# Optimization experiments

Hardware: AMD Instinct MI355X
Metric: run time of the kernel (lower is better)

The kernel has to match this reference:

```python
import jax, jax.numpy as jnp
import numpy as np

SENT_LEN, SENT_BATCH, WORD_LEN = 256, 64, 16
EMB, HID = 128, 256
CEMB, CHID = 64, 128
VOCAB, CVOCAB, TAGS = 50000, 128, 50


def setup_inputs() -> dict:
    key = jax.random.key(0)
    ks = jax.random.split(key, 14)
    s = 0.1  # param init scale, avoids gate saturation
    n = lambda k, shape: (jax.random.normal(k, shape, dtype=jnp.float32) * s)
    return {
        "sentences": jax.random.randint(ks[0], (SENT_LEN, SENT_BATCH), 0, VOCAB),
        "words": jax.random.randint(ks[1], (SENT_BATCH, WORD_LEN, SENT_LEN), 0, CVOCAB),
        "char_embedding_dim": CEMB,
        "char_hidden_dim": CHID,
        "word_emb": n(ks[2], (VOCAB, EMB)),
        "char_emb": n(ks[3], (CVOCAB, CEMB)),
        "Wih_c": n(ks[4], (4 * CHID, CEMB)),
        "Whh_c": n(ks[5], (4 * CHID, CHID)),
        "bih_c": n(ks[6], (4 * CHID,)),
        "bhh_c": n(ks[7], (4 * CHID,)),
        "Wih_w": n(ks[8], (4 * HID, EMB + CHID)),
        "Whh_w": n(ks[9], (4 * HID, HID)),
        "bih_w": n(ks[10], (4 * HID,)),
        "bhh_w": n(ks[11], (4 * HID,)),
        "W_tag": n(ks[12], (TAGS, HID)),
        "b_tag": n(ks[13], (TAGS,)),
    }


def _lstm_cell(h, c, x, Wih, Whh, b):
    # torch gate order: input, forget, cell(g), output
    gates = x @ Wih.T + h @ Whh.T + b
    i, f, g, o = jnp.split(gates, 4, axis=-1)
    c_new = jax.nn.sigmoid(f) * c + jax.nn.sigmoid(i) * jnp.tanh(g)
    h_new = jax.nn.sigmoid(o) * jnp.tanh(c_new)
    return h_new, c_new


def reference(sentences, words, char_embedding_dim, char_hidden_dim,
              word_emb, char_emb, Wih_c, Whh_c, bih_c, bhh_c,
              Wih_w, Whh_w, bih_w, bhh_w, W_tag, b_tag):
    sent_len, sent_batch = sentences.shape
    dt = word_emb.dtype

    embeds = word_emb[sentences]            # [T, B, EMB]
    ce = char_emb[words]                    # [B, WL, T, CEMB]

    # char LSTM: per sentence, seq=WL, batch=T; hidden carried ACROSS sentences
    b_c = bih_c + bhh_c

    def char_sentence(carry, sent_ce):      # sent_ce: [WL, T, CEMB]
        def step(hc, x):
            h, c = _lstm_cell(hc[0], hc[1], x, Wih_c, Whh_c, b_c)
            return (h, c), None
        carry, _ = jax.lax.scan(step, carry, sent_ce)
        return carry, carry[0]               # final h: [T, CHID]

    init_c = (jnp.zeros((sent_len, CHID), dt), jnp.zeros((sent_len, CHID), dt))
    _, char_finals = jax.lax.scan(char_sentence, init_c, ce)  # [B, T, CHID]
    char_finals = jnp.transpose(char_finals, (1, 0, 2))        # [T, B, CHID]

    x = jnp.concatenate([embeds, char_finals], axis=-1)        # [T, B, EMB+CHID]

    # word LSTM over time=T, batch=B
    b_w = bih_w + bhh_w

    def word_step(hc, xt):
        h, c = _lstm_cell(hc[0], hc[1], xt, Wih_w, Whh_w, b_w)
        return (h, c), h

    init_w = (jnp.zeros((sent_batch, HID), dt), jnp.zeros((sent_batch, HID), dt))
    _, lstm_out = jax.lax.scan(word_step, init_w, x)           # [T, B, HID]

    tag_space = lstm_out @ W_tag.T + b_tag                     # [T, B, TAGS]
    return jax.nn.log_softmax(tag_space, axis=-1)
```

## Files before the change

kernel.cpp:

```cpp
#include <hip/hip_runtime.h>
#include <hip/hip_bf16.h>
#include <cstdint>

#define SENT_LEN   256
#define SENT_BATCH 64
#define WORD_LEN   16
#define EMB        128
#define HID        256
#define CEMB       64
#define CHID       128
#define TAGS       50
#define K_IN       (EMB + CHID)
#define LOG2E      1.44269504f
#define N2LOG2E    -2.88539008f

typedef __attribute__((ext_vector_type(8))) short short8;
typedef __attribute__((ext_vector_type(4))) float f32x4;
typedef __attribute__((ext_vector_type(4))) int   i32x4;
typedef __attribute__((ext_vector_type(2))) long  lng2;

__device__ __forceinline__ float rcpf(float x) { return __builtin_amdgcn_rcpf(x); }
__device__ __forceinline__ float sig2(float xl) {
    return rcpf(1.f + __builtin_amdgcn_exp2f(-xl));
}
__device__ __forceinline__ float tanh2(float xl) {
    float e = __builtin_amdgcn_exp2f(-(xl + xl));
    return 2.f * rcpf(1.f + e) - 1.f;
}
__device__ __forceinline__ float lstm_act(float gi, float gf, float gg, float go, float& cst) {
    float c = sig2(gf) * cst + sig2(gi) * tanh2(gg);
    cst = c;
    float tc = 2.f * rcpf(1.f + __builtin_amdgcn_exp2f(N2LOG2E * c)) - 1.f;
    return sig2(go) * tc;
}
__device__ __forceinline__ float bf_lo(unsigned u) { return __uint_as_float(u << 16); }
__device__ __forceinline__ float bf_hi(unsigned u) { return __uint_as_float(u & 0xffff0000u); }
__device__ __forceinline__ unsigned short f2bfu(float f) {
    unsigned u = __float_as_uint(f);
    u += 0x7fff + ((u >> 16) & 1);
    return (unsigned short)(u >> 16);
}
__device__ __forceinline__ void block_sync_lds() {
    asm volatile("s_waitcnt lgkmcnt(0)\ns_barrier" ::: "memory");
}
__device__ __forceinline__ i32x4 mfma_i8_k64(lng2 a, lng2 b, i32x4 c) {
    c = __builtin_amdgcn_mfma_i32_16x16x32_i8(a.x, b.x, c, 0, 0, 0);
    return __builtin_amdgcn_mfma_i32_16x16x32_i8(a.y, b.y, c, 0, 0, 0);
}

__global__ void prep_char(const float* __restrict__ Wih_c, const float* __restrict__ char_emb,
                          const float* __restrict__ bih_c, const float* __restrict__ bhh_c,
                          float* __restrict__ pre8) {
    int ch = blockIdx.x;
    int g  = threadIdx.x;
    float acc = bih_c[g] + bhh_c[g];
    const float* w = Wih_c + g * CEMB;
    const float* e = char_emb + ch * CEMB;
#pragma unroll
    for (int k = 0; k < CEMB; k++) acc += w[k] * e[k];
    int gt = g >> 7, j = g & 127;
    pre8[((ch * 128) + j) * 4 + gt] = acc * LOG2E;
}

__global__ void prep_wq(const float* __restrict__ Whh_w, signed char* __restrict__ wq,
                        float* __restrict__ sw) {
    int g = blockIdx.x;
    int lane = threadIdx.x;
    float4 v = reinterpret_cast<const float4*>(Whh_w + (size_t)g * HID)[lane];
    float m = fmaxf(fmaxf(fabsf(v.x), fabsf(v.y)), fmaxf(fabsf(v.z), fabsf(v.w)));
#pragma unroll
    for (int off = 32; off; off >>= 1) m = fmaxf(m, __shfl_xor(m, off, 64));
    m = fmaxf(m, 1e-20f);
    float inv = 127.f / m;
    int q0 = __float2int_rn(v.x * inv), q1 = __float2int_rn(v.y * inv);
    int q2 = __float2int_rn(v.z * inv), q3 = __float2int_rn(v.w * inv);
    int packed = (q0 & 255) | ((q1 & 255) << 8) | ((q2 & 255) << 16) | ((q3 & 255) << 24);
    reinterpret_cast<int*>(wq)[g * 64 + lane] = packed;
    if (lane == 0) sw[g] = m / 127.f;
}

__global__ __launch_bounds__(512, 1) void char_lstm(
        const int* __restrict__ words, const float* __restrict__ Whh_c,
        const float* __restrict__ pre8, float* __restrict__ cf) {
    int t    = blockIdx.x;
    int tid  = threadIdx.x;
    int lane = tid & 63, w = tid >> 6;
    int l15  = lane & 15, lq = lane >> 4;
    int j    = w * 16 + l15;

    __shared__ __align__(16) signed char hv[2][128];

    lng2 bfr[4][2];
    float swl[4];
#pragma unroll
    for (int nt = 0; nt < 4; nt++) {
        const float* wr = Whh_c + (size_t)(nt * 128 + j) * CHID;
        float v[2][16];
        float m = 0.f;
#pragma unroll
        for (int kt = 0; kt < 2; kt++) {
#pragma unroll
            for (int q = 0; q < 4; q++) {
                float4 f = reinterpret_cast<const float4*>(wr + kt * 64 + lq * 16 + q * 4)[0];
                v[kt][q * 4 + 0] = f.x; v[kt][q * 4 + 1] = f.y;
                v[kt][q * 4 + 2] = f.z; v[kt][q * 4 + 3] = f.w;
            }
#pragma unroll
            for (int p = 0; p < 16; p++) m = fmaxf(m, fabsf(v[kt][p]));
        }
        m = fmaxf(m, __shfl_xor(m, 16, 64));
        m = fmaxf(m, __shfl_xor(m, 32, 64));
        m = fmaxf(m, 1e-20f);
        float inv = 127.f / m;
#pragma unroll
        for (int kt = 0; kt < 2; kt++) {
            unsigned long lo = 0, hi = 0;
#pragma unroll
            for (int p = 0; p < 8; p++) {
                lo |= (unsigned long)((unsigned)__float2int_rn(v[kt][p] * inv) & 255) << (8 * p);
                hi |= (unsigned long)((unsigned)__float2int_rn(v[kt][p + 8] * inv) & 255) << (8 * p);
            }
            lng2 bb; bb.x = (long)lo; bb.y = (long)hi;
            bfr[nt][kt] = bb;
        }
        swl[nt] = m * (LOG2E / (127.f * 127.f));
    }
    if (tid < 64) { reinterpret_cast<int*>(hv)[tid] = 0; }

    float cst = 0.f;
    const float4* pre4p = reinterpret_cast<const float4*>(pre8);
    int cid0 = words[t];
    int cid1 = words[SENT_LEN + t];
    float4 pr0 = pre4p[cid0 * 128 + j];
    float4 pr1 = pre4p[cid1 * 128 + j];
    int cidn0 = words[2 * SENT_LEN + t];
    int cidn1 = words[3 * SENT_LEN + t];
    __syncthreads();

    for (int u = 0; u < 512; u++) {
        float4 prn0 = pre4p[cidn0 * 128 + j];
        float4 prn1 = pre4p[cidn1 * 128 + j];
        cidn0 = words[(((u << 1) + 4) & 1023) * SENT_LEN + t];
        cidn1 = words[(((u << 1) + 5) & 1023) * SENT_LEN + t];

        {
            const lng2* hp = reinterpret_cast<const lng2*>(hv[0]);
            lng2 a0 = hp[lq];
            lng2 a1 = hp[4 + lq];
            i32x4 acc[4] = {};
#pragma unroll
            for (int nt = 0; nt < 4; nt++) {
                acc[nt] = mfma_i8_k64(a0, bfr[nt][0], acc[nt]);
                acc[nt] = mfma_i8_k64(a1, bfr[nt][1], acc[nt]);
            }
            float gi = (float)acc[0][0] * swl[0] + pr0.x;
            float gf = (float)acc[1][0] * swl[1] + pr0.y;
            float gg = (float)acc[2][0] * swl[2] + pr0.z;
            float go = (float)acc[3][0] * swl[3] + pr0.w;
            float h = lstm_act(gi, gf, gg, go, cst);
            if (lq == 0)
                hv[1][j] = (signed char)__float2int_rn(h * 127.f);
            block_sync_lds();
        }
        {
            const lng2* hp = reinterpret_cast<const lng2*>(hv[1]);
            lng2 a0 = hp[lq];
            lng2 a1 = hp[4 + lq];
            i32x4 acc[4] = {};
#pragma unroll
            for (int nt = 0; nt < 4; nt++) {
                acc[nt] = mfma_i8_k64(a0, bfr[nt][0], acc[nt]);
                acc[nt] = mfma_i8_k64(a1, bfr[nt][1], acc[nt]);
            }
            float gi = (float)acc[0][0] * swl[0] + pr1.x;
            float gf = (float)acc[1][0] * swl[1] + pr1.y;
            float gg = (float)acc[2][0] * swl[2] + pr1.z;
            float go = (float)acc[3][0] * swl[3] + pr1.w;
            float h = lstm_act(gi, gf, gg, go, cst);
            if (lq == 0) {
                hv[0][j] = (signed char)__float2int_rn(h * 127.f);
                if ((u & 7) == 7)
                    cf[((size_t)t * SENT_BATCH + (u >> 3)) * CHID + j] = h;
            }
            block_sync_lds();
        }
        pr0 = prn0; pr1 = prn1;
    }
}

#define XW_SEG 65
__global__ __launch_bounds__(256, 2) void xw_gemm(
        const int* __restrict__ sentences, const float* __restrict__ word_emb,
        const float* __restrict__ cf, const float* __restrict__ Wih_w,
        const float* __restrict__ bih_w, const float* __restrict__ bhh_w,
        uint2* __restrict__ xw8) {
    __shared__ short8 Apack[32 * XW_SEG];
    __shared__ short8 Bpack[32 * XW_SEG];
    __shared__ int sid_s[64];
    int tid = threadIdx.x;
    int j0 = blockIdx.x * 16;
    int row0 = blockIdx.y * 64;
    if (tid < 64) sid_s[tid] = sentences[row0 + tid];
    __syncthreads();

#pragma unroll
    for (int it = 0; it < 8; it++) {
        int idx = it * 256 + tid;
        int m = idx >> 5, k8 = idx & 31;
        int k = k8 * 8;
        int kt = k8 >> 2, lqs = k8 & 3;
        int lanes = (m & 15) + (lqs << 4);
        int seg = kt * 4 + (m >> 4);
        const float* asrc = (k < EMB)
            ? word_emb + (size_t)sid_s[m] * EMB + k
            : cf + (size_t)(row0 + m) * CHID + (k - EMB);
        float4 a0 = reinterpret_cast<const float4*>(asrc)[0];
        float4 a1 = reinterpret_cast<const float4*>(asrc)[1];
        short8 av;
        av[0] = (short)f2bfu(a0.x); av[1] = (short)f2bfu(a0.y);
        av[2] = (short)f2bfu(a0.z); av[3] = (short)f2bfu(a0.w);
        av[4] = (short)f2bfu(a1.x); av[5] = (short)f2bfu(a1.y);
        av[6] = (short)f2bfu(a1.z); av[7] = (short)f2bfu(a1.w);
        Apack[seg * XW_SEG + lanes] = av;
        const float* bsrc = Wih_w + (size_t)((m >> 4) * 256 + j0 + (m & 15)) * K_IN + k;
        float4 b0 = reinterpret_cast<const float4*>(bsrc)[0];
        float4 b1 = reinterpret_cast<const float4*>(bsrc)[1];
        short8 bv;
        bv[0] = (short)f2bfu(b0.x); bv[1] = (short)f2bfu(b0.y);
        bv[2] = (short)f2bfu(b0.z); bv[3] = (short)f2bfu(b0.w);
        bv[4] = (short)f2bfu(b1.x); bv[5] = (short)f2bfu(b1.y);
        bv[6] = (short)f2bfu(b1.z); bv[7] = (short)f2bfu(b1.w);
        Bpack[seg * XW_SEG + lanes] = bv;
    }
    __syncthreads();

    int lane = tid & 63, wv = tid >> 6, l15 = lane & 15, lq = lane >> 4;
    f32x4 acc[4] = {{0.f,0.f,0.f,0.f},{0.f,0.f,0.f,0.f},{0.f,0.f,0.f,0.f},{0.f,0.f,0.f,0.f}};
#pragma unroll
    for (int kt = 0; kt < 8; kt++) {
        short8 a = Apack[(kt * 4 + wv) * XW_SEG + lane];
#pragma unroll
        for (int nt = 0; nt < 4; nt++)
            acc[nt] = __builtin_amdgcn_mfma_f32_16x16x32_bf16(
                a, Bpack[(kt * 4 + nt) * XW_SEG + lane], acc[nt], 0, 0, 0);
    }
    float bb[4];
#pragma unroll
    for (int nt = 0; nt < 4; nt++)
        bb[nt] = bih_w[nt * 256 + j0 + l15] + bhh_w[nt * 256 + j0 + l15];
    int t = row0 >> 6;
#pragma unroll
    for (int r = 0; r < 4; r++) {
        int b = wv * 16 + lq * 4 + r;
        uint2 o;
        o.x = (unsigned)f2bfu((acc[0][r] + bb[0]) * LOG2E)
            | ((unsigned)f2bfu((acc[1][r] + bb[1]) * LOG2E) << 16);
        o.y = (unsigned)f2bfu((acc[2][r] + bb[2]) * LOG2E)
            | ((unsigned)f2bfu((acc[3][r] + bb[3]) * LOG2E) << 16);
        xw8[((size_t)b * SENT_LEN + t) * 256 + j0 + l15] = o;
    }
}

__global__ __launch_bounds__(1024, 1) void word_lstm(
        const uint2* __restrict__ xw8, const signed char* __restrict__ wq,
        const float* __restrict__ sw, float* __restrict__ h_out) {
    int b    = blockIdx.x;
    int tid  = threadIdx.x;
    int lane = tid & 63, w = tid >> 6;
    int l15  = lane & 15, lq = lane >> 4;
    int j    = w * 16 + l15;

    __shared__ __align__(16) signed char hv[2][256];

    lng2 bfr[4][4];
    float swl[4];
#pragma unroll
    for (int nt = 0; nt < 4; nt++) {
        int g = nt * 256 + j;
        swl[nt] = sw[g] * (LOG2E / 127.f);
#pragma unroll
        for (int kt = 0; kt < 4; kt++)
            bfr[nt][kt] = reinterpret_cast<const lng2*>(wq + (size_t)g * HID + kt * 64 + lq * 16)[0];
    }
    if (tid < 128) { reinterpret_cast<int*>(hv)[tid] = 0; }

    const uint2* xwb = xw8 + (size_t)b * SENT_LEN * 256;
    float cst = 0.f;
    uint2 xq0 = xwb[0 * 256 + j];
    uint2 xq1 = xwb[1 * 256 + j];
    uint2 xq2 = xwb[2 * 256 + j];
    uint2 xq3 = xwb[3 * 256 + j];
    __syncthreads();

    for (int u = 0; u < 128; u++) {
        uint2 xn0 = xwb[((((u << 1) + 4) & 255)) * 256 + j];
        uint2 xn1 = xwb[((((u << 1) + 5) & 255)) * 256 + j];

        {
            const lng2* hp = reinterpret_cast<const lng2*>(hv[0]);
            i32x4 acc[4] = {};
#pragma unroll
            for (int kt = 0; kt < 4; kt++) {
                lng2 a = hp[kt * 4 + lq];
#pragma unroll
                for (int nt = 0; nt < 4; nt++)
                    acc[nt] = mfma_i8_k64(a, bfr[nt][kt], acc[nt]);
            }
            float gi = (float)acc[0][0] * swl[0] + bf_lo(xq0.x);
            float gf = (float)acc[1][0] * swl[1] + bf_hi(xq0.x);
            float gg = (float)acc[2][0] * swl[2] + bf_lo(xq0.y);
            float go = (float)acc[3][0] * swl[3] + bf_hi(xq0.y);
            float h = lstm_act(gi, gf, gg, go, cst);
            if (lq == 0) {
                h_out[((size_t)(u << 1) * SENT_BATCH + b) * HID + j] = h;
                hv[1][j] = (signed char)__float2int_rn(h * 127.f);
            }
            block_sync_lds();
        }
        {
            const lng2* hp = reinterpret_cast<const lng2*>(hv[1]);
            i32x4 acc[4] = {};
#pragma unroll
            for (int kt = 0; kt < 4; kt++) {
                lng2 a = hp[kt * 4 + lq];
#pragma unroll
                for (int nt = 0; nt < 4; nt++)
                    acc[nt] = mfma_i8_k64(a, bfr[nt][kt], acc[nt]);
            }
            float gi = (float)acc[0][0] * swl[0] + bf_lo(xq1.x);
            float gf = (float)acc[1][0] * swl[1] + bf_hi(xq1.x);
            float gg = (float)acc[2][0] * swl[2] + bf_lo(xq1.y);
            float go = (float)acc[3][0] * swl[3] + bf_hi(xq1.y);
            float h = lstm_act(gi, gf, gg, go, cst);
            if (lq == 0) {
                h_out[((size_t)((u << 1) + 1) * SENT_BATCH + b) * HID + j] = h;
                hv[0][j] = (signed char)__float2int_rn(h * 127.f);
            }
            block_sync_lds();
        }
        xq0 = xq2; xq1 = xq3; xq2 = xn0; xq3 = xn1;
    }
}

__global__ __launch_bounds__(256) void tag_logsoftmax(
        const float* __restrict__ h_out, const float* __restrict__ W_tag,
        const float* __restrict__ b_tag, float* __restrict__ out) {
    __shared__ float wt_s[TAGS * 257];
    __shared__ float hr_s[4 * HID];
    int tid = threadIdx.x;
    int row0 = blockIdx.x * 4;
#pragma unroll 2
    for (int i = 0; i < TAGS; i++) wt_s[i * 257 + tid] = W_tag[i * HID + tid];
#pragma unroll
    for (int w = 0; w < 4; w++) hr_s[w * HID + tid] = h_out[(size_t)(row0 + w) * HID + tid];
    __syncthreads();

    int w = tid >> 6, l = tid & 63;
    float acc = 0.f;
    if (l < TAGS) {
        acc = b_tag[l];
        const float* hr = hr_s + w * HID;
        const float* wr = wt_s + l * 257;
#pragma unroll 4
        for (int k = 0; k < HID; k++) acc += hr[k] * wr[k];
    }
    float m = (l < TAGS) ? acc : -1e30f;
#pragma unroll
    for (int off = 32; off; off >>= 1) m = fmaxf(m, __shfl_xor(m, off, 64));
    float e = (l < TAGS) ? __builtin_amdgcn_exp2f((acc - m) * LOG2E) : 0.f;
    float ssum = e;
#pragma unroll
    for (int off = 32; off; off >>= 1) ssum += __shfl_xor(ssum, off, 64);
    float lse = m + __logf(ssum);
    if (l < TAGS) out[(size_t)(row0 + w) * TAGS + l] = acc - lse;
}

extern "C" void kernel_launch(void* const* d_in, const int* in_sizes, int n_in,
                              void* d_out, int out_size, void* d_ws, size_t ws_size,
                              hipStream_t stream) {
    (void)in_sizes; (void)n_in; (void)out_size; (void)ws_size;
    const int*   sentences = (const int*)d_in[0];
    const int*   words     = (const int*)d_in[1];
    const float* word_emb  = (const float*)d_in[4];
    const float* char_emb  = (const float*)d_in[5];
    const float* Wih_c     = (const float*)d_in[6];
    const float* Whh_c     = (const float*)d_in[7];
    const float* bih_c     = (const float*)d_in[8];
    const float* bhh_c     = (const float*)d_in[9];
    const float* Wih_w     = (const float*)d_in[10];
    const float* Whh_w     = (const float*)d_in[11];
    const float* bih_w     = (const float*)d_in[12];
    const float* bhh_w     = (const float*)d_in[13];
    const float* W_tag     = (const float*)d_in[14];
    const float* b_tag     = (const float*)d_in[15];
    float* out = (float*)d_out;

    char* ws = (char*)d_ws;
    size_t off = 0;
    float* pre8 = (float*)(ws + off);                 off += 128 * 512 * sizeof(float);
    signed char* wq = (signed char*)(ws + off);       off += 1024 * 256;
    float* sw = (float*)(ws + off);                   off += 1024 * sizeof(float);
    off = (off + 255) & ~(size_t)255;
    float* cf = (float*)(ws + off);                   off += (size_t)SENT_LEN * SENT_BATCH * CHID * sizeof(float);
    uint2* xw8 = (uint2*)(ws + off);                  off += (size_t)SENT_LEN * SENT_BATCH * 256 * sizeof(uint2);
    float* h_out = (float*)(ws + off);                off += (size_t)SENT_LEN * SENT_BATCH * HID * sizeof(float);

    hipLaunchKernelGGL(prep_char, dim3(128), dim3(512), 0, stream,
                       Wih_c, char_emb, bih_c, bhh_c, pre8);
    hipLaunchKernelGGL(prep_wq, dim3(1024), dim3(64), 0, stream, Whh_w, wq, sw);
    hipLaunchKernelGGL(char_lstm, dim3(256), dim3(512), 0, stream,
                       words, Whh_c, pre8, cf);
    hipLaunchKernelGGL(xw_gemm, dim3(16, 256), dim3(256), 0, stream,
                       sentences, word_emb, cf, Wih_w, bih_w, bhh_w, xw8);
    hipLaunchKernelGGL(word_lstm, dim3(SENT_BATCH), dim3(1024), 0, stream,
                       xw8, wq, sw, h_out);
    hipLaunchKernelGGL(tag_logsoftmax, dim3((SENT_LEN * SENT_BATCH) / 4), dim3(256), 0, stream,
                       h_out, W_tag, b_tag, out);
}
```

Before: 959.5 us.

## Replace char-LSTM MFMA recurrence with per-lane sdot4 gate rows and DPP broadcast

In the char LSTM recurrence, each lane now owns one gate row (gate type from lane&3) and holds its int8-quantized Whh row in registers. It computes the h·W dot product with sdot4 over hidden state read from LDS, replacing the 16x16 int8 MFMAs whose outputs were mostly unused. Each lane applies one activation, and the four gate values are shared among a lane quad with DPP quad-permute broadcasts. This cuts MFMA latency on the serial per-step critical path and removes redundant activation work, at the cost of 8 LDS vector reads per step and more register use.

```diff
diff --git a/kernel.cpp b/kernel.cpp
--- a/kernel.cpp
+++ b/kernel.cpp
@@ -47,6 +47,10 @@
     c = __builtin_amdgcn_mfma_i32_16x16x32_i8(a.x, b.x, c, 0, 0, 0);
     return __builtin_amdgcn_mfma_i32_16x16x32_i8(a.y, b.y, c, 0, 0, 0);
 }
+template<int Q> __device__ __forceinline__ float qbcast(float x) {
+    return __int_as_float(__builtin_amdgcn_mov_dpp(
+        __float_as_int(x), Q * 0x55, 0xF, 0xF, false));
+}
 
 __global__ void prep_char(const float* __restrict__ Wih_c, const float* __restrict__ char_emb,
                           const float* __restrict__ bih_c, const float* __restrict__ bhh_c,
@@ -85,106 +89,110 @@
     int t    = blockIdx.x;
     int tid  = threadIdx.x;
     int lane = tid & 63, w = tid >> 6;
-    int l15  = lane & 15, lq = lane >> 4;
-    int j    = w * 16 + l15;
+    int nt   = lane & 3;
+    int j    = w * 16 + (lane >> 2);
+    int g    = nt * 128 + j;
 
     __shared__ __align__(16) signed char hv[2][128];
 
-    lng2 bfr[4][2];
-    float swl[4];
-#pragma unroll
-    for (int nt = 0; nt < 4; nt++) {
-        const float* wr = Whh_c + (size_t)(nt * 128 + j) * CHID;
-        float v[2][16];
-        float m = 0.f;
-#pragma unroll
-        for (int kt = 0; kt < 2; kt++) {
-#pragma unroll
-            for (int q = 0; q < 4; q++) {
-                float4 f = reinterpret_cast<const float4*>(wr + kt * 64 + lq * 16 + q * 4)[0];
-                v[kt][q * 4 + 0] = f.x; v[kt][q * 4 + 1] = f.y;
-                v[kt][q * 4 + 2] = f.z; v[kt][q * 4 + 3] = f.w;
-            }
-#pragma unroll
-            for (int p = 0; p < 16; p++) m = fmaxf(m, fabsf(v[kt][p]));
-        }
-        m = fmaxf(m, __shfl_xor(m, 16, 64));
-        m = fmaxf(m, __shfl_xor(m, 32, 64));
-        m = fmaxf(m, 1e-20f);
-        float inv = 127.f / m;
-#pragma unroll
-        for (int kt = 0; kt < 2; kt++) {
-            unsigned long lo = 0, hi = 0;
-#pragma unroll
-            for (int p = 0; p < 8; p++) {
-                lo |= (unsigned long)((unsigned)__float2int_rn(v[kt][p] * inv) & 255) << (8 * p);
-                hi |= (unsigned long)((unsigned)__float2int_rn(v[kt][p + 8] * inv) & 255) << (8 * p);
-            }
-            lng2 bb; bb.x = (long)lo; bb.y = (long)hi;
-            bfr[nt][kt] = bb;
-        }
-        swl[nt] = m * (LOG2E / (127.f * 127.f));
-    }
+    const float4* wr = reinterpret_cast<const float4*>(Whh_c + (size_t)g * CHID);
+    float mx = 1e-20f;
+#pragma unroll
+    for (int q = 0; q < 32; q++) {
+        float4 f = wr[q];
+        mx = fmaxf(mx, fmaxf(fmaxf(fabsf(f.x), fabsf(f.y)), fmaxf(fabsf(f.z), fabsf(f.w))));
+    }
+    float inv = 127.f / mx;
+    int wqr[32];
+#pragma unroll
+    for (int q = 0; q < 32; q++) {
+        float4 f = wr[q];
+        wqr[q] = (__float2int_rn(f.x * inv) & 255)
+               | ((__float2int_rn(f.y * inv) & 255) << 8)
+               | ((__float2int_rn(f.z * inv) & 255) << 16)
+               | ((__float2int_rn(f.w * inv) & 255) << 24);
+    }
+    float swl = mx * (LOG2E / (127.f * 127.f));
+
+    float s_e = (nt == 2) ? -2.f : -1.f;
+    float m_a = (nt == 2) ?  2.f :  1.f;
+    float b_a = (nt == 2) ? -1.f :  0.f;
+
     if (tid < 64) { reinterpret_cast<int*>(hv)[tid] = 0; }
 
     float cst = 0.f;
-    const float4* pre4p = reinterpret_cast<const float4*>(pre8);
     int cid0 = words[t];
     int cid1 = words[SENT_LEN + t];
-    float4 pr0 = pre4p[cid0 * 128 + j];
-    float4 pr1 = pre4p[cid1 * 128 + j];
+    float pl0 = pre8[(size_t)cid0 * 512 + tid];
+    float pl1 = pre8[(size_t)cid1 * 512 + tid];
     int cidn0 = words[2 * SENT_LEN + t];
     int cidn1 = words[3 * SENT_LEN + t];
     __syncthreads();
 
     for (int u = 0; u < 512; u++) {
-        float4 prn0 = pre4p[cidn0 * 128 + j];
-        float4 prn1 = pre4p[cidn1 * 128 + j];
+        float pn0 = pre8[(size_t)cidn0 * 512 + tid];
+        float pn1 = pre8[(size_t)cidn1 * 512 + tid];
         cidn0 = words[(((u << 1) + 4) & 1023) * SENT_LEN + t];
         cidn1 = words[(((u << 1) + 5) & 1023) * SENT_LEN + t];
 
         {
-            const lng2* hp = reinterpret_cast<const lng2*>(hv[0]);
-            lng2 a0 = hp[lq];
-            lng2 a1 = hp[4 + lq];
-            i32x4 acc[4] = {};
-#pragma unroll
-            for (int nt = 0; nt < 4; nt++) {
-                acc[nt] = mfma_i8_k64(a0, bfr[nt][0], acc[nt]);
-                acc[nt] = mfma_i8_k64(a1, bfr[nt][1], acc[nt]);
-            }
-            float gi = (float)acc[0][0] * swl[0] + pr0.x;
-            float gf = (float)acc[1][0] * swl[1] + pr0.y;
-            float gg = (float)acc[2][0] * swl[2] + pr0.z;
-            float go = (float)acc[3][0] * swl[3] + pr0.w;
-            float h = lstm_act(gi, gf, gg, go, cst);
-            if (lq == 0)
+            const i32x4* hp = reinterpret_cast<const i32x4*>(hv[0]);
+            int a0 = 0, a1 = 0, a2 = 0, a3 = 0;
+#pragma unroll
+            for (int q = 0; q < 8; q++) {
+                i32x4 hq = hp[q];
+                a0 = __builtin_amdgcn_sdot4(hq.x, wqr[q * 4 + 0], a0, false);
+                a1 = __builtin_amdgcn_sdot4(hq.y, wqr[q * 4 + 1], a1, false);
+                a2 = __builtin_amdgcn_sdot4(hq.z, wqr[q * 4 + 2], a2, false);
+                a3 = __builtin_amdgcn_sdot4(hq.w, wqr[q * 4 + 3], a3, false);
+            }
+            int acc = (a0 + a1) + (a2 + a3);
+            float gv = (float)acc * swl + pl0;
+            float e  = __builtin_amdgcn_exp2f(s_e * gv);
+            float av = m_a * rcpf(1.f + e) + b_a;
+            float qi = qbcast<0>(av);
+            float qf = qbcast<1>(av);
+            float qg = qbcast<2>(av);
+            float qo = qbcast<3>(av);
+            float c  = qf * cst + qi * qg;
+            cst = c;
+            float tc = 2.f * rcpf(1.f + __builtin_amdgcn_exp2f(N2LOG2E * c)) - 1.f;
+            float h  = qo * tc;
+            if (nt == 0)
                 hv[1][j] = (signed char)__float2int_rn(h * 127.f);
             block_sync_lds();
         }
         {
-            const lng2* hp = reinterpret_cast<const lng2*>(hv[1]);
-            lng2 a0 = hp[lq];
-            lng2 a1 = hp[4 + lq];
-            i32x4 acc[4] = {};
-#pragma unroll
-            for (int nt = 0; nt < 4; nt++) {
-                acc[nt] = mfma_i8_k64(a0, bfr[nt][0], acc[nt]);
-                acc[nt] = mfma_i8_k64(a1, bfr[nt][1], acc[nt]);
-            }
-            float gi = (float)acc[0][0] * swl[0] + pr1.x;
-            float gf = (float)acc[1][0] * swl[1] + pr1.y;
-            float gg = (float)acc[2][0] * swl[2] + pr1.z;
-            float go = (float)acc[3][0] * swl[3] + pr1.w;
-            float h = lstm_act(gi, gf, gg, go, cst);
-            if (lq == 0) {
+            const i32x4* hp = reinterpret_cast<const i32x4*>(hv[1]);
+            int a0 = 0, a1 = 0, a2 = 0, a3 = 0;
+#pragma unroll
+            for (int q = 0; q < 8; q++) {
+                i32x4 hq = hp[q];
+                a0 = __builtin_amdgcn_sdot4(hq.x, wqr[q * 4 + 0], a0, false);
+                a1 = __builtin_amdgcn_sdot4(hq.y, wqr[q * 4 + 1], a1, false);
+                a2 = __builtin_amdgcn_sdot4(hq.z, wqr[q * 4 + 2], a2, false);
+                a3 = __builtin_amdgcn_sdot4(hq.w, wqr[q * 4 + 3], a3, false);
+            }
+            int acc = (a0 + a1) + (a2 + a3);
+            float gv = (float)acc * swl + pl1;
+            float e  = __builtin_amdgcn_exp2f(s_e * gv);
+            float av = m_a * rcpf(1.f + e) + b_a;
+            float qi = qbcast<0>(av);
+            float qf = qbcast<1>(av);
+            float qg = qbcast<2>(av);
+            float qo = qbcast<3>(av);
+            float c  = qf * cst + qi * qg;
+            cst = c;
+            float tc = 2.f * rcpf(1.f + __builtin_amdgcn_exp2f(N2LOG2E * c)) - 1.f;
+            float h  = qo * tc;
+            if (nt == 0) {
                 hv[0][j] = (signed char)__float2int_rn(h * 127.f);
                 if ((u & 7) == 7)
                     cf[((size_t)t * SENT_BATCH + (u >> 3)) * CHID + j] = h;
             }
             block_sync_lds();
         }
-        pr0 = prn0; pr1 = prn1;
+        pl0 = pn0; pl1 = pn1;
     }
 }
 
```

Result: faster. 938.7 us (-2.2%).
